# Kernel tuning notes

Hardware: AMD Instinct MI355X
Metric: run time of the kernel (lower is better)

The kernel has to match this reference:

```python
import jax, jax.numpy as jnp
import numpy as np

B, T, IN, H, S, L = 64, 512, 512, 512, 128, 2
ALPHA = 0.5  # default alpha in SCLSTM.forward


def setup_inputs() -> dict:
    key = jax.random.key(0)
    ks = jax.random.split(key, 9)
    p = lambda k, shape: jax.random.normal(k, shape, jnp.float32) * 0.05
    return {
        "inputs": jax.random.normal(ks[0], (B, T, IN), jnp.float32),
        "W_ir": p(ks[1], (S, IN)),
        "b_ir": p(ks[2], (S,)),
        "W_hr": p(ks[3], (S, L * H)),
        "b_hr": p(ks[4], (S,)),
        "gW": p(ks[5], (L, 4 * H, IN + H)),  # per-layer gate Linear (input_size==hidden_size)
        "gb": p(ks[6], (L, 4 * H)),
        "sW": p(ks[7], (L, H, S)),           # per-layer slot_linear
        "sb": p(ks[8], (L, H)),
    }


def reference(inputs, W_ir, b_ir, W_hr, b_hr, gW, gb, sW, sb):
    bsize = inputs.shape[0]
    h0 = jnp.zeros((bsize, L, H), inputs.dtype)
    c0 = jnp.zeros((bsize, L, H), inputs.dtype)
    s0 = jnp.zeros((bsize, S), inputs.dtype)

    def step(carry, x_t):  # x_t: (B, IN)
        h, c, s = carry
        # reading gate over flattened hidden states of all layers
        r = jax.nn.sigmoid(x_t @ W_ir.T + b_ir
                           + ALPHA * (h.reshape(bsize, L * H) @ W_hr.T + b_hr))
        s = s * r  # slot state update
        cur = x_t
        hs, cs = [], []
        for l in range(L):  # fixed small layer count
            gates = jnp.concatenate([cur, h[:, l]], axis=1) @ gW[l].T + gb[l]
            i_g, f_g, o_g, info = jnp.split(gates, 4, axis=1)
            slot_info = jnp.tanh(s @ sW[l].T + sb[l])
            c_n = (jax.nn.sigmoid(f_g) * c[:, l]
                   + jax.nn.sigmoid(i_g) * jnp.tanh(info) + slot_info)
            h_n = jax.nn.sigmoid(o_g) * jnp.tanh(c_n)
            hs.append(h_n); cs.append(c_n)
            cur = h_n  # skip_connections=False, dropout=0
        h = jnp.stack(hs, axis=1)
        c = jnp.stack(cs, axis=1)
        return (h, c, s), hs[-1]  # output is last layer's hidden state

    (ht, ct, st), outs = jax.lax.scan(step, (h0, c0, s0), jnp.swapaxes(inputs, 0, 1))
    outputs = jnp.swapaxes(outs, 0, 1)  # (B, T, H)
    return outputs, (ht, ct), st
```

## Files before the change

### kernel.cpp

```cpp
#include <hip/hip_runtime.h>


typedef unsigned short ushort;
typedef unsigned long long u64;
using bfrag = __attribute__((ext_vector_type(8))) short;
using cfrag = __attribute__((ext_vector_type(4))) float;
using i4    = __attribute__((ext_vector_type(4))) int;

constexpr int NBLK = 256, NTHR = 512;
constexpr int Bsz = 64, Tt = 512, Hsz = 512;
constexpr int D0 = 8;
constexpr int DP = 2;

constexpr long long OUT_HT = (long long)Bsz * Tt * Hsz;
constexpr long long OUT_CT = OUT_HT + (long long)Bsz * 2 * Hsz;
constexpr long long OUT_ST = OUT_CT + (long long)Bsz * 2 * Hsz;

constexpr int WS_SLOTS_A = 0;
constexpr int WS_SLOTS_B = 8 * 1024;
constexpr int WS_PROG_A  = 16 * 1024;
constexpr int WS_PROG_B  = 17 * 1024;
constexpr int WS_XCC     = 18 * 1024;
constexpr int WS_RING0   = 64 * 1024;
constexpr int WS_RING1   = WS_RING0 + D0 * Bsz * Hsz * 2;
constexpr int WS_RINGA   = WS_RING1 + DP * Bsz * Hsz * 2;
constexpr int WS_TOTAL   = WS_RINGA + DP * Bsz * Hsz * 2;

__global__ __launch_bounds__(256) void sclstm_init(float* __restrict__ ws,
                                                   float* __restrict__ out) {
    int i = blockIdx.x * blockDim.x + threadIdx.x, st = gridDim.x * blockDim.x;
    for (int k = i; k < WS_TOTAL / 4; k += st) ws[k] = 0.f;
    for (int k = i; k < Bsz * 128; k += st) out[OUT_ST + k] = 0.f;
}

__device__ __forceinline__ float sigm(float x) { return 1.f / (1.f + __expf(-x)); }
__device__ __forceinline__ float ftanh(float x) {
    float e = __expf(2.f * x);
    return 1.f - 2.f / (e + 1.f);
}
__device__ __forceinline__ ushort f2bf(float f) {
    unsigned u = __builtin_bit_cast(unsigned, f);
    u += 0x7FFFu + ((u >> 16) & 1u);
    return (ushort)(u >> 16);
}
__device__ __forceinline__ int aload(const int* p) {
    return __hip_atomic_load(p, __ATOMIC_RELAXED, __HIP_MEMORY_SCOPE_AGENT);
}
__device__ __forceinline__ int load_sc0(const int* p) {
    int v;
    asm volatile("global_load_dword %0, %1, off sc0\n\ts_waitcnt vmcnt(0)"
                 : "=v"(v) : "v"(p) : "memory");
    return v;
}
__device__ __forceinline__ void spin_agent(const int* p, int v) {
    int it = 0;
    while (aload(p) < v) {
        __builtin_amdgcn_s_sleep(1);
        if (((++it) & 1023) == 0)
            __builtin_amdgcn_fence(__ATOMIC_ACQUIRE, "agent");
    }
}
__device__ __forceinline__ void spin_f(const int* p, int v, int fast) {
    if (fast) {
        int it = 0;
        while (load_sc0(p) < v) {
            __builtin_amdgcn_s_sleep(1);
            if (((++it) & 63) == 0)
                __builtin_amdgcn_fence(__ATOMIC_ACQUIRE, "agent");
        }
    } else {
        spin_agent(p, v);
    }
}
__device__ __forceinline__ void st_flag(int* p, int v, int fast) {
    if (fast) __hip_atomic_store(p, v, __ATOMIC_RELAXED, __HIP_MEMORY_SCOPE_WORKGROUP);
    else      __hip_atomic_store(p, v, __ATOMIC_RELAXED, __HIP_MEMORY_SCOPE_AGENT);
}
__device__ __forceinline__ void st_h(ushort* p, ushort v, int fast) {
    if (fast) __hip_atomic_store(p, v, __ATOMIC_RELAXED, __HIP_MEMORY_SCOPE_WORKGROUP);
    else      __hip_atomic_store(p, v, __ATOMIC_RELAXED, __HIP_MEMORY_SCOPE_AGENT);
}
__device__ __forceinline__ bfrag pack2(u64 q0, u64 q1) {
    bfrag v;
    v[0]=(short)(ushort)(q0); v[1]=(short)(ushort)(q0 >> 16);
    v[2]=(short)(ushort)(q0 >> 32); v[3]=(short)(ushort)(q0 >> 48);
    v[4]=(short)(ushort)(q1); v[5]=(short)(ushort)(q1 >> 16);
    v[6]=(short)(ushort)(q1 >> 32); v[7]=(short)(ushort)(q1 >> 48);
    return v;
}

__global__ __launch_bounds__(NTHR, 2) void sclstm_main(
    const float* __restrict__ inputs,
    const float* __restrict__ gW,
    const float* __restrict__ gb,
    const float* __restrict__ sbias,
    float* __restrict__ out,
    float* __restrict__ ws)
{
    __shared__ __attribute__((aligned(16))) ushort frag_lds[32 * 512];
    __shared__ float part_lds[64 * 17 * 2];
    __shared__ int fast_sh;

    char* wsb = (char*)ws;
    const int tid = threadIdx.x, blk = blockIdx.x;
    const int setB = blk & 1;
    const int grp = (blk >> 1) & 3;
    const int myidx = blk >> 3;
    const int L = setB;
    const int b0 = grp * 16, m0 = myidx * 16;

    int* slots     = (int*)(wsb + (setB ? WS_SLOTS_B : WS_SLOTS_A)) + grp * 32 * 16;
    int* prog_self = (int*)(wsb + (setB ? WS_PROG_B : WS_PROG_A)) + grp * 16;
    int* prog_up   = (int*)(wsb + WS_PROG_A) + grp * 16;
    int* prog_down = (int*)(wsb + WS_PROG_B) + grp * 16;
    ushort* ring0 = (ushort*)(wsb + WS_RING0);
    ushort* ring1 = (ushort*)(wsb + WS_RING1);
    ushort* ringA = (ushort*)(wsb + WS_RINGA);
    ushort* ring_own = setB ? ring1 : ringA;

    const int lane = tid & 63, wave = tid >> 6;
    const int tau = wave & 3, g = wave >> 2;
    const int q = lane >> 4, lm = lane & 15;

    bfrag wv[16];
    {
        const int grow = tau * 512 + m0 + lm;
        const float* wrow = gW + ((size_t)L * 2048 + grow) * 1024 + g * 512 + q * 8;
        #pragma unroll
        for (int j = 0; j < 16; ++j) {
            const float* src = wrow + j * 32;
            float4 a = *(const float4*)src, b = *(const float4*)(src + 4);
            bfrag v;
            v[0]=(short)f2bf(a.x); v[1]=(short)f2bf(a.y); v[2]=(short)f2bf(a.z); v[3]=(short)f2bf(a.w);
            v[4]=(short)f2bf(b.x); v[5]=(short)f2bf(b.y); v[6]=(short)f2bf(b.z); v[7]=(short)f2bf(b.w);
            wv[j] = v;
        }
    }
    float bias4[4] = {0.f, 0.f, 0.f, 0.f};
    float slotc = 0.f, c = 0.f;
    if (tid < 256) {
        const int mi = tid & 15;
        #pragma unroll
        for (int tg = 0; tg < 4; ++tg) bias4[tg] = gb[L * 2048 + tg * 512 + m0 + mi];
        slotc = ftanh(sbias[L * 512 + m0 + mi]);
    }

    int fast;
    {
        unsigned xcc = (unsigned)__builtin_amdgcn_s_getreg((31 << 11) | 20) & 0xFu;
        int* xarr = (int*)(wsb + WS_XCC) + (setB * 4 + grp) * 32 * 16;
        if (tid == 0) {
            __hip_atomic_store(xarr + myidx * 16, (int)xcc + 1,
                               __ATOMIC_RELAXED, __HIP_MEMORY_SCOPE_AGENT);
            int ok = 1, ref = 0;
            for (int i = 0; i < 32; ++i) {
                int v;
                while ((v = aload(xarr + i * 16)) == 0) __builtin_amdgcn_s_sleep(2);
                if (i == 0) ref = v; else ok &= (v == ref);
            }
            fast_sh = ok;
        }
        __syncthreads();
        fast = fast_sh;
    }

    auto stage_nonrec = [&](int tt) {
        #pragma unroll
        for (int it = 0; it < 2; ++it) {
            const int ks = it * 8 + wave;
            bfrag v;
            if (!setB) {
                const float* xs = inputs + ((size_t)(b0 + lm) * Tt + tt) * 512 + ks * 32 + q * 8;
                float4 a = *(const float4*)xs, b = *(const float4*)(xs + 4);
                v[0]=(short)f2bf(a.x); v[1]=(short)f2bf(a.y); v[2]=(short)f2bf(a.z); v[3]=(short)f2bf(a.w);
                v[4]=(short)f2bf(b.x); v[5]=(short)f2bf(b.y); v[6]=(short)f2bf(b.z); v[7]=(short)f2bf(b.w);
            } else {
                const ushort* hs = ring0 + (size_t)(tt & (D0 - 1)) * (Bsz * Hsz)
                                 + (b0 + lm) * 512 + ks * 32 + q * 8;
                u64 q0 = __hip_atomic_load((const u64*)hs, __ATOMIC_RELAXED, __HIP_MEMORY_SCOPE_AGENT);
                u64 q1 = __hip_atomic_load((const u64*)(hs + 4), __ATOMIC_RELAXED, __HIP_MEMORY_SCOPE_AGENT);
                v = pack2(q0, q1);
            }
            *(bfrag*)&frag_lds[ks * 512 + lane * 8] = v;
        }
    };

    if (setB) {
        if (tid == 0) spin_agent(prog_up, 1);
        __syncthreads();
    }
    stage_nonrec(0);

    for (int t = 0; t < Tt; ++t) {
        const int rsp = (t - 1) & (DP - 1), rsc = t & (DP - 1);

        {
            const ushort* hb_ = ring_own + (size_t)rsp * (Bsz * Hsz) + (b0 + lm) * 512 + q * 8;
            const ushort* p0 = hb_ + wave * 32;
            const ushort* p1 = hb_ + (wave + 8) * 32;
            bfrag v0, v1;
            if (fast) {
                i4 w0, w1;
                asm volatile(
                    "global_load_dwordx4 %0, %2, off sc0\n\t"
                    "global_load_dwordx4 %1, %3, off sc0\n\t"
                    "s_waitcnt vmcnt(0)"
                    : "=&v"(w0), "=&v"(w1) : "v"(p0), "v"(p1) : "memory");
                v0 = __builtin_bit_cast(bfrag, w0);
                v1 = __builtin_bit_cast(bfrag, w1);
            } else {
                u64 a0 = __hip_atomic_load((const u64*)p0, __ATOMIC_RELAXED, __HIP_MEMORY_SCOPE_AGENT);
                u64 a1 = __hip_atomic_load((const u64*)(p0 + 4), __ATOMIC_RELAXED, __HIP_MEMORY_SCOPE_AGENT);
                u64 c0 = __hip_atomic_load((const u64*)p1, __ATOMIC_RELAXED, __HIP_MEMORY_SCOPE_AGENT);
                u64 c1 = __hip_atomic_load((const u64*)(p1 + 4), __ATOMIC_RELAXED, __HIP_MEMORY_SCOPE_AGENT);
                v0 = pack2(a0, a1); v1 = pack2(c0, c1);
            }
            *(bfrag*)&frag_lds[(16 + wave) * 512 + lane * 8] = v0;
            *(bfrag*)&frag_lds[(24 + wave) * 512 + lane * 8] = v1;
        }
        __syncthreads();

        cfrag C0 = {0.f, 0.f, 0.f, 0.f}, C1 = {0.f, 0.f, 0.f, 0.f};
        #pragma unroll
        for (int j = 0; j < 16; j += 2) {
            bfrag Bf0 = *(const bfrag*)&frag_lds[(g * 16 + j) * 512 + lane * 8];
            C0 = __builtin_amdgcn_mfma_f32_16x16x32_bf16(wv[j], Bf0, C0, 0, 0, 0);
            bfrag Bf1 = *(const bfrag*)&frag_lds[(g * 16 + j + 1) * 512 + lane * 8];
            C1 = __builtin_amdgcn_mfma_f32_16x16x32_bf16(wv[j + 1], Bf1, C1, 0, 0, 0);
        }
        #pragma unroll
        for (int reg = 0; reg < 4; ++reg) {
            const int lrow = tau * 16 + q * 4 + reg;
            part_lds[(lrow * 17 + lm) * 2 + g] = C0[reg] + C1[reg];
        }
        __syncthreads();

        float hn = 0.f, cn = 0.f;
        if (tid < 256) {
            const int mi = tid & 15, b3 = tid >> 4;
            float gs[4];
            #pragma unroll
            for (int tg = 0; tg < 4; ++tg) {
                float2 p = *(const float2*)&part_lds[((tg * 16 + mi) * 17 + b3) * 2];
                gs[tg] = p.x + p.y + bias4[tg];
            }
            cn = sigm(gs[1]) * c + sigm(gs[0]) * ftanh(gs[3]) + slotc;
            hn = sigm(gs[2]) * ftanh(cn);
            c = cn;
            const ushort hb16 = f2bf(hn);
            const size_t poff = (size_t)(b0 + b3) * 512 + m0 + mi;
            st_h(ring_own + (size_t)rsc * (Bsz * Hsz) + poff, hb16, fast);
            if (!setB)
                __hip_atomic_store(ring0 + (size_t)(t & (D0 - 1)) * (Bsz * Hsz) + poff,
                                   hb16, __ATOMIC_RELAXED, __HIP_MEMORY_SCOPE_AGENT);
        }
        __syncthreads();
        if (tid == 0) st_flag(&slots[myidx * 16], t + 1, fast);

        if (t + 1 < Tt) {
            if (setB) {
                if (tid == 0) spin_agent(prog_up, t + 2);
                __syncthreads();
            } else if ((t + 1) >= D0 && tid == 0) {
                spin_agent(prog_down, t + 2 - D0);
            }
            stage_nonrec(t + 1);
        }
        if (tid < 256) {
            const int mi = tid & 15, b3 = tid >> 4;
            if (setB)
                out[((size_t)(b0 + b3) * Tt + t) * Hsz + m0 + mi] = hn;
            if (t == Tt - 1) {
                out[OUT_HT + (size_t)(b0 + b3) * 1024 + L * 512 + m0 + mi] = hn;
                out[OUT_CT + (size_t)(b0 + b3) * 1024 + L * 512 + m0 + mi] = cn;
            }
        }
        if (tid < 32) spin_f(&slots[tid * 16], t + 1, fast);
        if (myidx == 0 && tid == 0)
            __hip_atomic_store(prog_self, t + 1, __ATOMIC_RELAXED, __HIP_MEMORY_SCOPE_AGENT);
        __syncthreads();
    }
}

extern "C" void kernel_launch(void* const* d_in, const int* in_sizes, int n_in,
                              void* d_out, int out_size, void* d_ws, size_t ws_size,
                              hipStream_t stream) {
    (void)in_sizes; (void)n_in; (void)out_size; (void)ws_size;
    const float* inputs = (const float*)d_in[0];
    const float* gW = (const float*)d_in[5];
    const float* gb = (const float*)d_in[6];
    const float* sbias = (const float*)d_in[8];
    float* out = (float*)d_out;
    float* ws = (float*)d_ws;

    hipLaunchKernelGGL(sclstm_init, dim3(256), dim3(256), 0, stream, ws, out);
    hipLaunchKernelGGL(sclstm_main, dim3(NBLK), dim3(NTHR), 0, stream,
                       inputs, gW, gb, sbias, out, ws);
}
```

Measured before the change: 1.824 ms.

## Halve block count with 32 hidden units per block and deferred cross-layer writes

Each block now computes 32 hidden units instead of 16, holding two sets of weight fragments and issuing four MFMA chains. That halves the grid to 128 blocks and the per-group barrier fan-in to 16 participants. Layer-0 writes to the cross-layer ring and layer-1 output stores are deferred to the start of the next step. Next-step inputs are prefetched into registers during the MFMA phase, and the syncthreads calls are replaced by raw s_barrier with explicit waitcnt. These changes aim to cut synchronisation and staging latency on the sequential critical path, at the cost of more registers per thread and more complex progress and flag logic.

```diff
diff --git a/kernel.cpp b/kernel.cpp
--- a/kernel.cpp
+++ b/kernel.cpp
@@ -2,12 +2,13 @@
 
 
 typedef unsigned short ushort;
+typedef unsigned int uint;
 typedef unsigned long long u64;
 using bfrag = __attribute__((ext_vector_type(8))) short;
 using cfrag = __attribute__((ext_vector_type(4))) float;
 using i4    = __attribute__((ext_vector_type(4))) int;
 
-constexpr int NBLK = 256, NTHR = 512;
+constexpr int NBLK = 128, NTHR = 512;
 constexpr int Bsz = 64, Tt = 512, Hsz = 512;
 constexpr int D0 = 8;
 constexpr int DP = 2;
@@ -76,10 +77,6 @@
     if (fast) __hip_atomic_store(p, v, __ATOMIC_RELAXED, __HIP_MEMORY_SCOPE_WORKGROUP);
     else      __hip_atomic_store(p, v, __ATOMIC_RELAXED, __HIP_MEMORY_SCOPE_AGENT);
 }
-__device__ __forceinline__ void st_h(ushort* p, ushort v, int fast) {
-    if (fast) __hip_atomic_store(p, v, __ATOMIC_RELAXED, __HIP_MEMORY_SCOPE_WORKGROUP);
-    else      __hip_atomic_store(p, v, __ATOMIC_RELAXED, __HIP_MEMORY_SCOPE_AGENT);
-}
 __device__ __forceinline__ bfrag pack2(u64 q0, u64 q1) {
     bfrag v;
     v[0]=(short)(ushort)(q0); v[1]=(short)(ushort)(q0 >> 16);
@@ -87,6 +84,25 @@
     v[4]=(short)(ushort)(q1); v[5]=(short)(ushort)(q1 >> 16);
     v[6]=(short)(ushort)(q1 >> 32); v[7]=(short)(ushort)(q1 >> 48);
     return v;
+}
+__device__ __forceinline__ bfrag packf(float4 a, float4 b) {
+    bfrag v;
+    v[0]=(short)f2bf(a.x); v[1]=(short)f2bf(a.y); v[2]=(short)f2bf(a.z); v[3]=(short)f2bf(a.w);
+    v[4]=(short)f2bf(b.x); v[5]=(short)f2bf(b.y); v[6]=(short)f2bf(b.z); v[7]=(short)f2bf(b.w);
+    return v;
+}
+__device__ __forceinline__ void bar_lgkm() {
+    asm volatile("s_waitcnt lgkmcnt(0)" ::: "memory");
+    __builtin_amdgcn_sched_barrier(0);
+    __builtin_amdgcn_s_barrier();
+}
+__device__ __forceinline__ void bar_vm0() {
+    asm volatile("s_waitcnt vmcnt(0) lgkmcnt(0)" ::: "memory");
+    __builtin_amdgcn_sched_barrier(0);
+    __builtin_amdgcn_s_barrier();
+}
+__device__ __forceinline__ void bar_raw() {
+    __builtin_amdgcn_s_barrier();
 }
 
 __global__ __launch_bounds__(NTHR, 2) void sclstm_main(
@@ -98,18 +114,19 @@
     float* __restrict__ ws)
 {
     __shared__ __attribute__((aligned(16))) ushort frag_lds[32 * 512];
-    __shared__ float part_lds[64 * 17 * 2];
+    __shared__ float part_lds[128 * 17 * 2];
     __shared__ int fast_sh;
 
     char* wsb = (char*)ws;
     const int tid = threadIdx.x, blk = blockIdx.x;
-    const int setB = blk & 1;
-    const int grp = (blk >> 1) & 3;
+    const int group = blk & 7;
+    const int setB = group & 1;
+    const int grp  = group >> 1;
     const int myidx = blk >> 3;
     const int L = setB;
-    const int b0 = grp * 16, m0 = myidx * 16;
-
-    int* slots     = (int*)(wsb + (setB ? WS_SLOTS_B : WS_SLOTS_A)) + grp * 32 * 16;
+    const int b0 = grp * 16, m0 = myidx * 32;
+
+    int* slots     = (int*)(wsb + (setB ? WS_SLOTS_B : WS_SLOTS_A)) + grp * 16 * 16;
     int* prog_self = (int*)(wsb + (setB ? WS_PROG_B : WS_PROG_A)) + grp * 16;
     int* prog_up   = (int*)(wsb + WS_PROG_A) + grp * 16;
     int* prog_down = (int*)(wsb + WS_PROG_B) + grp * 16;
@@ -122,38 +139,40 @@
     const int tau = wave & 3, g = wave >> 2;
     const int q = lane >> 4, lm = lane & 15;
 
-    bfrag wv[16];
-    {
-        const int grow = tau * 512 + m0 + lm;
+    bfrag wv[2][16];
+    #pragma unroll
+    for (int m = 0; m < 2; ++m) {
+        const int grow = tau * 512 + m0 + m * 16 + lm;
         const float* wrow = gW + ((size_t)L * 2048 + grow) * 1024 + g * 512 + q * 8;
         #pragma unroll
         for (int j = 0; j < 16; ++j) {
             const float* src = wrow + j * 32;
-            float4 a = *(const float4*)src, b = *(const float4*)(src + 4);
-            bfrag v;
-            v[0]=(short)f2bf(a.x); v[1]=(short)f2bf(a.y); v[2]=(short)f2bf(a.z); v[3]=(short)f2bf(a.w);
-            v[4]=(short)f2bf(b.x); v[5]=(short)f2bf(b.y); v[6]=(short)f2bf(b.z); v[7]=(short)f2bf(b.w);
-            wv[j] = v;
-        }
-    }
-    float bias4[4] = {0.f, 0.f, 0.f, 0.f};
-    float slotc = 0.f, c = 0.f;
+            wv[m][j] = packf(*(const float4*)src, *(const float4*)(src + 4));
+        }
+    }
+    const int mp = tid & 15, b3 = tid >> 4;
+    float bias2[4][2], slot2[2], cc2[2] = {0.f, 0.f};
+    float hnf2[2] = {0.f, 0.f};
+    uint hq_hold = 0;
     if (tid < 256) {
-        const int mi = tid & 15;
         #pragma unroll
-        for (int tg = 0; tg < 4; ++tg) bias4[tg] = gb[L * 2048 + tg * 512 + m0 + mi];
-        slotc = ftanh(sbias[L * 512 + m0 + mi]);
+        for (int k = 0; k < 2; ++k) {
+            #pragma unroll
+            for (int tg = 0; tg < 4; ++tg)
+                bias2[tg][k] = gb[L * 2048 + tg * 512 + m0 + 2 * mp + k];
+            slot2[k] = ftanh(sbias[L * 512 + m0 + 2 * mp + k]);
+        }
     }
 
     int fast;
     {
         unsigned xcc = (unsigned)__builtin_amdgcn_s_getreg((31 << 11) | 20) & 0xFu;
-        int* xarr = (int*)(wsb + WS_XCC) + (setB * 4 + grp) * 32 * 16;
+        int* xarr = (int*)(wsb + WS_XCC) + group * 16 * 16;
         if (tid == 0) {
             __hip_atomic_store(xarr + myidx * 16, (int)xcc + 1,
                                __ATOMIC_RELAXED, __HIP_MEMORY_SCOPE_AGENT);
             int ok = 1, ref = 0;
-            for (int i = 0; i < 32; ++i) {
+            for (int i = 0; i < 16; ++i) {
                 int v;
                 while ((v = aload(xarr + i * 16)) == 0) __builtin_amdgcn_s_sleep(2);
                 if (i == 0) ref = v; else ok &= (v == ref);
@@ -164,32 +183,29 @@
         fast = fast_sh;
     }
 
-    auto stage_nonrec = [&](int tt) {
-        #pragma unroll
-        for (int it = 0; it < 2; ++it) {
-            const int ks = it * 8 + wave;
-            bfrag v;
-            if (!setB) {
-                const float* xs = inputs + ((size_t)(b0 + lm) * Tt + tt) * 512 + ks * 32 + q * 8;
-                float4 a = *(const float4*)xs, b = *(const float4*)(xs + 4);
-                v[0]=(short)f2bf(a.x); v[1]=(short)f2bf(a.y); v[2]=(short)f2bf(a.z); v[3]=(short)f2bf(a.w);
-                v[4]=(short)f2bf(b.x); v[5]=(short)f2bf(b.y); v[6]=(short)f2bf(b.z); v[7]=(short)f2bf(b.w);
-            } else {
-                const ushort* hs = ring0 + (size_t)(tt & (D0 - 1)) * (Bsz * Hsz)
-                                 + (b0 + lm) * 512 + ks * 32 + q * 8;
-                u64 q0 = __hip_atomic_load((const u64*)hs, __ATOMIC_RELAXED, __HIP_MEMORY_SCOPE_AGENT);
-                u64 q1 = __hip_atomic_load((const u64*)(hs + 4), __ATOMIC_RELAXED, __HIP_MEMORY_SCOPE_AGENT);
-                v = pack2(q0, q1);
-            }
-            *(bfrag*)&frag_lds[ks * 512 + lane * 8] = v;
-        }
-    };
-
     if (setB) {
         if (tid == 0) spin_agent(prog_up, 1);
         __syncthreads();
     }
-    stage_nonrec(0);
+    #pragma unroll
+    for (int it = 0; it < 2; ++it) {
+        const int r = wave * 2 + it;
+        bfrag v;
+        if (!setB) {
+            const float* xs = inputs + ((size_t)(b0 + lm) * Tt + 0) * 512 + r * 32 + q * 8;
+            v = packf(*(const float4*)xs, *(const float4*)(xs + 4));
+        } else {
+            const ushort* hs = ring0 + (b0 + lm) * 512 + r * 32 + q * 8;
+            u64 q0 = __hip_atomic_load((const u64*)hs, __ATOMIC_RELAXED, __HIP_MEMORY_SCOPE_AGENT);
+            u64 q1 = __hip_atomic_load((const u64*)(hs + 4), __ATOMIC_RELAXED, __HIP_MEMORY_SCOPE_AGENT);
+            v = pack2(q0, q1);
+        }
+        *(bfrag*)&frag_lds[r * 512 + lane * 8] = v;
+    }
+
+    int cach_down = 0;
+    float4 pxa[3][2];
+    u64 phb[3][2];
 
     for (int t = 0; t < Tt; ++t) {
         const int rsp = (t - 1) & (DP - 1), rsc = t & (DP - 1);
@@ -218,67 +234,137 @@
             *(bfrag*)&frag_lds[(16 + wave) * 512 + lane * 8] = v0;
             *(bfrag*)&frag_lds[(24 + wave) * 512 + lane * 8] = v1;
         }
-        __syncthreads();
-
-        cfrag C0 = {0.f, 0.f, 0.f, 0.f}, C1 = {0.f, 0.f, 0.f, 0.f};
+        int pv_now = 0x7fffffff;
+        if (t > 0 && tid < 256) {
+            if (!setB) {
+                const int tgt = t - 8;
+                if (tgt > 0 && cach_down < tgt) {
+                    do { __builtin_amdgcn_s_sleep(1); cach_down = aload(prog_down); }
+                    while (cach_down < tgt);
+                }
+                ushort* rp = ring0 + (size_t)((t - 1) & (D0 - 1)) * (Bsz * Hsz)
+                           + (b0 + b3) * 512 + m0 + 2 * mp;
+                __hip_atomic_store((uint*)rp, hq_hold, __ATOMIC_RELAXED, __HIP_MEMORY_SCOPE_AGENT);
+            } else {
+                float2 o = {hnf2[0], hnf2[1]};
+                *(float2*)(out + ((size_t)(b0 + b3) * Tt + (t - 1)) * Hsz + m0 + 2 * mp) = o;
+            }
+        }
+        if (setB && wave > 0 && t + 1 < Tt)
+            pv_now = aload(prog_up);
+
+        bar_lgkm();
+
+        if (wave > 0 && t + 1 < Tt) {
+            if (setB && pv_now < t + 2) spin_agent(prog_up, t + 2);
+            #pragma unroll
+            for (int it = 0; it < 3; ++it) {
+                const int r = wave - 1 + it * 7;
+                if (r < 16) {
+                    if (!setB) {
+                        const float* xs = inputs + ((size_t)(b0 + lm) * Tt + (t + 1)) * 512 + r * 32 + q * 8;
+                        pxa[it][0] = *(const float4*)xs;
+                        pxa[it][1] = *(const float4*)(xs + 4);
+                    } else {
+                        const ushort* hs = ring0 + (size_t)((t + 1) & (D0 - 1)) * (Bsz * Hsz)
+                                         + (b0 + lm) * 512 + r * 32 + q * 8;
+                        phb[it][0] = __hip_atomic_load((const u64*)hs, __ATOMIC_RELAXED, __HIP_MEMORY_SCOPE_AGENT);
+                        phb[it][1] = __hip_atomic_load((const u64*)(hs + 4), __ATOMIC_RELAXED, __HIP_MEMORY_SCOPE_AGENT);
+                    }
+                }
+            }
+            asm volatile("" ::: "memory");
+        }
+
+        cfrag C00 = {0,0,0,0}, C01 = {0,0,0,0}, C10 = {0,0,0,0}, C11 = {0,0,0,0};
         #pragma unroll
         for (int j = 0; j < 16; j += 2) {
             bfrag Bf0 = *(const bfrag*)&frag_lds[(g * 16 + j) * 512 + lane * 8];
-            C0 = __builtin_amdgcn_mfma_f32_16x16x32_bf16(wv[j], Bf0, C0, 0, 0, 0);
             bfrag Bf1 = *(const bfrag*)&frag_lds[(g * 16 + j + 1) * 512 + lane * 8];
-            C1 = __builtin_amdgcn_mfma_f32_16x16x32_bf16(wv[j + 1], Bf1, C1, 0, 0, 0);
+            C00 = __builtin_amdgcn_mfma_f32_16x16x32_bf16(wv[0][j],     Bf0, C00, 0, 0, 0);
+            C10 = __builtin_amdgcn_mfma_f32_16x16x32_bf16(wv[1][j],     Bf0, C10, 0, 0, 0);
+            C01 = __builtin_amdgcn_mfma_f32_16x16x32_bf16(wv[0][j + 1], Bf1, C01, 0, 0, 0);
+            C11 = __builtin_amdgcn_mfma_f32_16x16x32_bf16(wv[1][j + 1], Bf1, C11, 0, 0, 0);
         }
         #pragma unroll
         for (int reg = 0; reg < 4; ++reg) {
-            const int lrow = tau * 16 + q * 4 + reg;
-            part_lds[(lrow * 17 + lm) * 2 + g] = C0[reg] + C1[reg];
-        }
-        __syncthreads();
-
-        float hn = 0.f, cn = 0.f;
+            const int r0 = tau * 32 + q * 4 + reg;
+            part_lds[(r0 * 17 + lm) * 2 + g] = C00[reg] + C01[reg];
+            part_lds[((r0 + 16) * 17 + lm) * 2 + g] = C10[reg] + C11[reg];
+        }
+        bar_lgkm();
+
         if (tid < 256) {
-            const int mi = tid & 15, b3 = tid >> 4;
-            float gs[4];
             #pragma unroll
-            for (int tg = 0; tg < 4; ++tg) {
-                float2 p = *(const float2*)&part_lds[((tg * 16 + mi) * 17 + b3) * 2];
-                gs[tg] = p.x + p.y + bias4[tg];
-            }
-            cn = sigm(gs[1]) * c + sigm(gs[0]) * ftanh(gs[3]) + slotc;
-            hn = sigm(gs[2]) * ftanh(cn);
-            c = cn;
-            const ushort hb16 = f2bf(hn);
-            const size_t poff = (size_t)(b0 + b3) * 512 + m0 + mi;
-            st_h(ring_own + (size_t)rsc * (Bsz * Hsz) + poff, hb16, fast);
-            if (!setB)
-                __hip_atomic_store(ring0 + (size_t)(t & (D0 - 1)) * (Bsz * Hsz) + poff,
-                                   hb16, __ATOMIC_RELAXED, __HIP_MEMORY_SCOPE_AGENT);
-        }
-        __syncthreads();
+            for (int k = 0; k < 2; ++k) {
+                const int fi = 2 * mp + k;
+                float gs[4];
+                #pragma unroll
+                for (int tg = 0; tg < 4; ++tg) {
+                    float2 p = *(const float2*)&part_lds[((tg * 32 + fi) * 17 + b3) * 2];
+                    gs[tg] = p.x + p.y + bias2[tg][k];
+                }
+                float cn = sigm(gs[1]) * cc2[k] + sigm(gs[0]) * ftanh(gs[3]) + slot2[k];
+                float hn = sigm(gs[2]) * ftanh(cn);
+                cc2[k] = cn; hnf2[k] = hn;
+            }
+            hq_hold = (uint)f2bf(hnf2[0]) | ((uint)f2bf(hnf2[1]) << 16);
+            ushort* rp = ring_own + (size_t)rsc * (Bsz * Hsz) + (b0 + b3) * 512 + m0 + 2 * mp;
+            if (fast) *(uint*)rp = hq_hold;
+            else __hip_atomic_store((uint*)rp, hq_hold, __ATOMIC_RELAXED, __HIP_MEMORY_SCOPE_AGENT);
+        }
+        bar_vm0();
         if (tid == 0) st_flag(&slots[myidx * 16], t + 1, fast);
 
-        if (t + 1 < Tt) {
-            if (setB) {
-                if (tid == 0) spin_agent(prog_up, t + 2);
-                __syncthreads();
-            } else if ((t + 1) >= D0 && tid == 0) {
-                spin_agent(prog_down, t + 2 - D0);
-            }
-            stage_nonrec(t + 1);
-        }
+        if (wave > 0) {
+            if (t + 1 < Tt) {
+                #pragma unroll
+                for (int it = 0; it < 3; ++it) {
+                    const int r = wave - 1 + it * 7;
+                    if (r < 16) {
+                        bfrag v = setB ? pack2(phb[it][0], phb[it][1])
+                                       : packf(pxa[it][0], pxa[it][1]);
+                        *(bfrag*)&frag_lds[r * 512 + lane * 8] = v;
+                    }
+                }
+            }
+        } else {
+            if (lane < 16) spin_f(&slots[lane * 16], t + 1, fast);
+            if (myidx == 0 && lane == 0)
+                __hip_atomic_store(prog_self, setB ? t + 1 : t,
+                                   __ATOMIC_RELAXED, __HIP_MEMORY_SCOPE_AGENT);
+        }
+        bar_raw();
+    }
+
+    if (!setB) {
         if (tid < 256) {
-            const int mi = tid & 15, b3 = tid >> 4;
-            if (setB)
-                out[((size_t)(b0 + b3) * Tt + t) * Hsz + m0 + mi] = hn;
-            if (t == Tt - 1) {
-                out[OUT_HT + (size_t)(b0 + b3) * 1024 + L * 512 + m0 + mi] = hn;
-                out[OUT_CT + (size_t)(b0 + b3) * 1024 + L * 512 + m0 + mi] = cn;
-            }
-        }
-        if (tid < 32) spin_f(&slots[tid * 16], t + 1, fast);
+            const int tgt = Tt - 8;
+            if (cach_down < tgt) {
+                do { __builtin_amdgcn_s_sleep(1); cach_down = aload(prog_down); }
+                while (cach_down < tgt);
+            }
+            ushort* rp = ring0 + (size_t)((Tt - 1) & (D0 - 1)) * (Bsz * Hsz)
+                       + (b0 + b3) * 512 + m0 + 2 * mp;
+            __hip_atomic_store((uint*)rp, hq_hold, __ATOMIC_RELAXED, __HIP_MEMORY_SCOPE_AGENT);
+        }
+        bar_vm0();
+        if (tid == 0) st_flag(&slots[myidx * 16], Tt + 1, fast);
+        if (wave == 0 && lane < 16) spin_f(&slots[lane * 16], Tt + 1, fast);
         if (myidx == 0 && tid == 0)
-            __hip_atomic_store(prog_self, t + 1, __ATOMIC_RELAXED, __HIP_MEMORY_SCOPE_AGENT);
-        __syncthreads();
+            __hip_atomic_store(prog_self, Tt, __ATOMIC_RELAXED, __HIP_MEMORY_SCOPE_AGENT);
+        if (tid < 256) {
+            float2 oh = {hnf2[0], hnf2[1]}, oc = {cc2[0], cc2[1]};
+            *(float2*)(out + OUT_HT + (size_t)(b0 + b3) * 1024 + 0 * 512 + m0 + 2 * mp) = oh;
+            *(float2*)(out + OUT_CT + (size_t)(b0 + b3) * 1024 + 0 * 512 + m0 + 2 * mp) = oc;
+        }
+    } else {
+        if (tid < 256) {
+            float2 oh = {hnf2[0], hnf2[1]}, oc = {cc2[0], cc2[1]};
+            *(float2*)(out + ((size_t)(b0 + b3) * Tt + (Tt - 1)) * Hsz + m0 + 2 * mp) = oh;
+            *(float2*)(out + OUT_HT + (size_t)(b0 + b3) * 1024 + 512 + m0 + 2 * mp) = oh;
+            *(float2*)(out + OUT_CT + (size_t)(b0 + b3) * 1024 + 512 + m0 + 2 * mp) = oc;
+        }
     }
 }
 
```

After: 5.169 ms. 183% more time.

## Prefetch next-step inputs in idle waves during gate compute, cache progress flag

Applied to the files above, without the earlier changes.

Waves 4-7, which sit idle during the elementwise gate update, now issue next-timestep input or ring0 loads into registers before that phase and write them to LDS afterwards. Waves 0-3 no longer do any staging. The layer-1 set only prefetches when the upstream progress flag is already far enough, and otherwise falls back to a per-wave spin plus direct staging. The downstream progress check caches the last value seen, which avoids redundant atomic loads. Slot flags move to new workspace offsets and the launch bound drops to one block per CU, giving more registers for the prefetch buffers.

```diff
diff --git a/kernel.cpp b/kernel.cpp
--- a/kernel.cpp
+++ b/kernel.cpp
@@ -2,6 +2,7 @@
 
 
 typedef unsigned short ushort;
+typedef unsigned int uint;
 typedef unsigned long long u64;
 using bfrag = __attribute__((ext_vector_type(8))) short;
 using cfrag = __attribute__((ext_vector_type(4))) float;
@@ -16,15 +17,15 @@
 constexpr long long OUT_CT = OUT_HT + (long long)Bsz * 2 * Hsz;
 constexpr long long OUT_ST = OUT_CT + (long long)Bsz * 2 * Hsz;
 
-constexpr int WS_SLOTS_A = 0;
-constexpr int WS_SLOTS_B = 8 * 1024;
-constexpr int WS_PROG_A  = 16 * 1024;
-constexpr int WS_PROG_B  = 17 * 1024;
-constexpr int WS_XCC     = 18 * 1024;
-constexpr int WS_RING0   = 64 * 1024;
-constexpr int WS_RING1   = WS_RING0 + D0 * Bsz * Hsz * 2;
-constexpr int WS_RINGA   = WS_RING1 + DP * Bsz * Hsz * 2;
-constexpr int WS_TOTAL   = WS_RINGA + DP * Bsz * Hsz * 2;
+constexpr int WS_PROG_A = 16 * 1024;
+constexpr int WS_PROG_B = 17 * 1024;
+constexpr int WS_XCC    = 18 * 1024;
+constexpr int WS_SLOTS_A = 40 * 1024;
+constexpr int WS_SLOTS_B = 48 * 1024;
+constexpr int WS_RING0  = 64 * 1024;
+constexpr int WS_RING1  = WS_RING0 + D0 * Bsz * Hsz * 2;
+constexpr int WS_RINGA  = WS_RING1 + DP * Bsz * Hsz * 2;
+constexpr int WS_TOTAL  = WS_RINGA + DP * Bsz * Hsz * 2;
 
 __global__ __launch_bounds__(256) void sclstm_init(float* __restrict__ ws,
                                                    float* __restrict__ out) {
@@ -88,8 +89,14 @@
     v[6]=(short)(ushort)(q1 >> 32); v[7]=(short)(ushort)(q1 >> 48);
     return v;
 }
-
-__global__ __launch_bounds__(NTHR, 2) void sclstm_main(
+__device__ __forceinline__ bfrag packf(float4 a, float4 b) {
+    bfrag v;
+    v[0]=(short)f2bf(a.x); v[1]=(short)f2bf(a.y); v[2]=(short)f2bf(a.z); v[3]=(short)f2bf(a.w);
+    v[4]=(short)f2bf(b.x); v[5]=(short)f2bf(b.y); v[6]=(short)f2bf(b.z); v[7]=(short)f2bf(b.w);
+    return v;
+}
+
+__global__ __launch_bounds__(NTHR, 1) void sclstm_main(
     const float* __restrict__ inputs,
     const float* __restrict__ gW,
     const float* __restrict__ gb,
@@ -129,11 +136,7 @@
         #pragma unroll
         for (int j = 0; j < 16; ++j) {
             const float* src = wrow + j * 32;
-            float4 a = *(const float4*)src, b = *(const float4*)(src + 4);
-            bfrag v;
-            v[0]=(short)f2bf(a.x); v[1]=(short)f2bf(a.y); v[2]=(short)f2bf(a.z); v[3]=(short)f2bf(a.w);
-            v[4]=(short)f2bf(b.x); v[5]=(short)f2bf(b.y); v[6]=(short)f2bf(b.z); v[7]=(short)f2bf(b.w);
-            wv[j] = v;
+            wv[j] = packf(*(const float4*)src, *(const float4*)(src + 4));
         }
     }
     float bias4[4] = {0.f, 0.f, 0.f, 0.f};
@@ -164,32 +167,31 @@
         fast = fast_sh;
     }
 
-    auto stage_nonrec = [&](int tt) {
-        #pragma unroll
-        for (int it = 0; it < 2; ++it) {
-            const int ks = it * 8 + wave;
-            bfrag v;
-            if (!setB) {
-                const float* xs = inputs + ((size_t)(b0 + lm) * Tt + tt) * 512 + ks * 32 + q * 8;
-                float4 a = *(const float4*)xs, b = *(const float4*)(xs + 4);
-                v[0]=(short)f2bf(a.x); v[1]=(short)f2bf(a.y); v[2]=(short)f2bf(a.z); v[3]=(short)f2bf(a.w);
-                v[4]=(short)f2bf(b.x); v[5]=(short)f2bf(b.y); v[6]=(short)f2bf(b.z); v[7]=(short)f2bf(b.w);
-            } else {
-                const ushort* hs = ring0 + (size_t)(tt & (D0 - 1)) * (Bsz * Hsz)
-                                 + (b0 + lm) * 512 + ks * 32 + q * 8;
-                u64 q0 = __hip_atomic_load((const u64*)hs, __ATOMIC_RELAXED, __HIP_MEMORY_SCOPE_AGENT);
-                u64 q1 = __hip_atomic_load((const u64*)(hs + 4), __ATOMIC_RELAXED, __HIP_MEMORY_SCOPE_AGENT);
-                v = pack2(q0, q1);
-            }
-            *(bfrag*)&frag_lds[ks * 512 + lane * 8] = v;
-        }
+    auto stage_row = [&](int r, int tt) {
+        bfrag v;
+        if (!setB) {
+            const float* xs = inputs + ((size_t)(b0 + lm) * Tt + tt) * 512 + r * 32 + q * 8;
+            v = packf(*(const float4*)xs, *(const float4*)(xs + 4));
+        } else {
+            const ushort* hs = ring0 + (size_t)(tt & (D0 - 1)) * (Bsz * Hsz)
+                             + (b0 + lm) * 512 + r * 32 + q * 8;
+            u64 q0 = __hip_atomic_load((const u64*)hs, __ATOMIC_RELAXED, __HIP_MEMORY_SCOPE_AGENT);
+            u64 q1 = __hip_atomic_load((const u64*)(hs + 4), __ATOMIC_RELAXED, __HIP_MEMORY_SCOPE_AGENT);
+            v = pack2(q0, q1);
+        }
+        *(bfrag*)&frag_lds[r * 512 + lane * 8] = v;
     };
 
     if (setB) {
         if (tid == 0) spin_agent(prog_up, 1);
         __syncthreads();
     }
-    stage_nonrec(0);
+    stage_row(wave * 2, 0);
+    stage_row(wave * 2 + 1, 0);
+
+    int cach_down = 0;
+    float4 pxa[4][2];
+    u64 phb[4][2];
 
     for (int t = 0; t < Tt; ++t) {
         const int rsp = (t - 1) & (DP - 1), rsc = t & (DP - 1);
@@ -235,6 +237,30 @@
         }
         __syncthreads();
 
+        int havepf = 0;
+        if (wave >= 4 && t + 1 < Tt) {
+            if (!setB) {
+                #pragma unroll
+                for (int it = 0; it < 4; ++it) {
+                    const int r = (wave - 4) * 4 + it;
+                    const float* xs = inputs + ((size_t)(b0 + lm) * Tt + (t + 1)) * 512 + r * 32 + q * 8;
+                    pxa[it][0] = *(const float4*)xs;
+                    pxa[it][1] = *(const float4*)(xs + 4);
+                }
+                havepf = 1;
+            } else if (aload(prog_up) >= t + 2) {
+                #pragma unroll
+                for (int it = 0; it < 4; ++it) {
+                    const int r = (wave - 4) * 4 + it;
+                    const ushort* hs = ring0 + (size_t)((t + 1) & (D0 - 1)) * (Bsz * Hsz)
+                                     + (b0 + lm) * 512 + r * 32 + q * 8;
+                    phb[it][0] = __hip_atomic_load((const u64*)hs, __ATOMIC_RELAXED, __HIP_MEMORY_SCOPE_AGENT);
+                    phb[it][1] = __hip_atomic_load((const u64*)(hs + 4), __ATOMIC_RELAXED, __HIP_MEMORY_SCOPE_AGENT);
+                }
+                havepf = 1;
+            }
+        }
+
         float hn = 0.f, cn = 0.f;
         if (tid < 256) {
             const int mi = tid & 15, b3 = tid >> 4;
@@ -255,16 +281,35 @@
                                    hb16, __ATOMIC_RELAXED, __HIP_MEMORY_SCOPE_AGENT);
         }
         __syncthreads();
-        if (tid == 0) st_flag(&slots[myidx * 16], t + 1, fast);
+        if (tid == 0)
+            st_flag(&slots[myidx * 16], t + 1, fast);
 
         if (t + 1 < Tt) {
-            if (setB) {
-                if (tid == 0) spin_agent(prog_up, t + 2);
-                __syncthreads();
-            } else if ((t + 1) >= D0 && tid == 0) {
-                spin_agent(prog_down, t + 2 - D0);
-            }
-            stage_nonrec(t + 1);
+            if (wave >= 4) {
+                if (havepf) {
+                    #pragma unroll
+                    for (int it = 0; it < 4; ++it) {
+                        const int r = (wave - 4) * 4 + it;
+                        bfrag v = setB ? pack2(phb[it][0], phb[it][1])
+                                       : packf(pxa[it][0], pxa[it][1]);
+                        *(bfrag*)&frag_lds[r * 512 + lane * 8] = v;
+                    }
+                } else {
+                    spin_agent(prog_up, t + 2);
+                    #pragma unroll
+                    for (int it = 0; it < 4; ++it)
+                        stage_row((wave - 4) * 4 + it, t + 1);
+                }
+            } else if (!setB && (t + 1) >= D0 && tid == 0) {
+                const int tgt = t + 2 - D0;
+                if (cach_down < tgt) {
+                    cach_down = aload(prog_down);
+                    while (cach_down < tgt) {
+                        __builtin_amdgcn_s_sleep(1);
+                        cach_down = aload(prog_down);
+                    }
+                }
+            }
         }
         if (tid < 256) {
             const int mi = tid & 15, b3 = tid >> 4;
@@ -277,7 +322,8 @@
         }
         if (tid < 32) spin_f(&slots[tid * 16], t + 1, fast);
         if (myidx == 0 && tid == 0)
-            __hip_atomic_store(prog_self, t + 1, __ATOMIC_RELAXED, __HIP_MEMORY_SCOPE_AGENT);
+            __hip_atomic_store(prog_self, t + 1,
+                               __ATOMIC_RELAXED, __HIP_MEMORY_SCOPE_AGENT);
         __syncthreads();
     }
 }
```

Result: slower. 5.131 ms (+181.3%).

## Prefetch next-step layer inputs before MFMA to overlap global latency

Applied to the files above, without the earlier changes.

Loads of the next timestep's non-recurrent operand are now issued before the per-step MFMA and gate math: raw inputs for layer 0, and ring0 hidden states for layer 1. They are held in registers and packed to LDS only after the step completes. Layer-1 blocks cache the last observed upstream progress value, so they skip the spin-plus-barrier when the producer is already far enough ahead, and fall back to the old spin path otherwise. This is meant to hide global-memory latency on the serial recurrence critical path, at the cost of extra live registers for the prefetch buffers.

```diff
diff --git a/kernel.cpp b/kernel.cpp
--- a/kernel.cpp
+++ b/kernel.cpp
@@ -60,6 +60,16 @@
             __builtin_amdgcn_fence(__ATOMIC_ACQUIRE, "agent");
     }
 }
+__device__ __forceinline__ int spin_cap(const int* p, int v) {
+    int x = aload(p), it = 0;
+    while (x < v) {
+        __builtin_amdgcn_s_sleep(1);
+        if (((++it) & 1023) == 0)
+            __builtin_amdgcn_fence(__ATOMIC_ACQUIRE, "agent");
+        x = aload(p);
+    }
+    return x;
+}
 __device__ __forceinline__ void spin_f(const int* p, int v, int fast) {
     if (fast) {
         int it = 0;
@@ -86,6 +96,12 @@
     v[2]=(short)(ushort)(q0 >> 32); v[3]=(short)(ushort)(q0 >> 48);
     v[4]=(short)(ushort)(q1); v[5]=(short)(ushort)(q1 >> 16);
     v[6]=(short)(ushort)(q1 >> 32); v[7]=(short)(ushort)(q1 >> 48);
+    return v;
+}
+__device__ __forceinline__ bfrag packf(float4 a, float4 b) {
+    bfrag v;
+    v[0]=(short)f2bf(a.x); v[1]=(short)f2bf(a.y); v[2]=(short)f2bf(a.z); v[3]=(short)f2bf(a.w);
+    v[4]=(short)f2bf(b.x); v[5]=(short)f2bf(b.y); v[6]=(short)f2bf(b.z); v[7]=(short)f2bf(b.w);
     return v;
 }
 
@@ -100,6 +116,7 @@
     __shared__ __attribute__((aligned(16))) ushort frag_lds[32 * 512];
     __shared__ float part_lds[64 * 17 * 2];
     __shared__ int fast_sh;
+    __shared__ int pv_sh;
 
     char* wsb = (char*)ws;
     const int tid = threadIdx.x, blk = blockIdx.x;
@@ -129,11 +146,7 @@
         #pragma unroll
         for (int j = 0; j < 16; ++j) {
             const float* src = wrow + j * 32;
-            float4 a = *(const float4*)src, b = *(const float4*)(src + 4);
-            bfrag v;
-            v[0]=(short)f2bf(a.x); v[1]=(short)f2bf(a.y); v[2]=(short)f2bf(a.z); v[3]=(short)f2bf(a.w);
-            v[4]=(short)f2bf(b.x); v[5]=(short)f2bf(b.y); v[6]=(short)f2bf(b.z); v[7]=(short)f2bf(b.w);
-            wv[j] = v;
+            wv[j] = packf(*(const float4*)src, *(const float4*)(src + 4));
         }
     }
     float bias4[4] = {0.f, 0.f, 0.f, 0.f};
@@ -164,32 +177,27 @@
         fast = fast_sh;
     }
 
-    auto stage_nonrec = [&](int tt) {
-        #pragma unroll
-        for (int it = 0; it < 2; ++it) {
-            const int ks = it * 8 + wave;
-            bfrag v;
-            if (!setB) {
-                const float* xs = inputs + ((size_t)(b0 + lm) * Tt + tt) * 512 + ks * 32 + q * 8;
-                float4 a = *(const float4*)xs, b = *(const float4*)(xs + 4);
-                v[0]=(short)f2bf(a.x); v[1]=(short)f2bf(a.y); v[2]=(short)f2bf(a.z); v[3]=(short)f2bf(a.w);
-                v[4]=(short)f2bf(b.x); v[5]=(short)f2bf(b.y); v[6]=(short)f2bf(b.z); v[7]=(short)f2bf(b.w);
-            } else {
-                const ushort* hs = ring0 + (size_t)(tt & (D0 - 1)) * (Bsz * Hsz)
-                                 + (b0 + lm) * 512 + ks * 32 + q * 8;
-                u64 q0 = __hip_atomic_load((const u64*)hs, __ATOMIC_RELAXED, __HIP_MEMORY_SCOPE_AGENT);
-                u64 q1 = __hip_atomic_load((const u64*)(hs + 4), __ATOMIC_RELAXED, __HIP_MEMORY_SCOPE_AGENT);
-                v = pack2(q0, q1);
-            }
-            *(bfrag*)&frag_lds[ks * 512 + lane * 8] = v;
-        }
+    auto stage_row = [&](int r, int tt) {
+        bfrag v;
+        if (!setB) {
+            const float* xs = inputs + ((size_t)(b0 + lm) * Tt + tt) * 512 + r * 32 + q * 8;
+            v = packf(*(const float4*)xs, *(const float4*)(xs + 4));
+        } else {
+            const ushort* hs = ring0 + (size_t)(tt & (D0 - 1)) * (Bsz * Hsz)
+                             + (b0 + lm) * 512 + r * 32 + q * 8;
+            u64 q0 = __hip_atomic_load((const u64*)hs, __ATOMIC_RELAXED, __HIP_MEMORY_SCOPE_AGENT);
+            u64 q1 = __hip_atomic_load((const u64*)(hs + 4), __ATOMIC_RELAXED, __HIP_MEMORY_SCOPE_AGENT);
+            v = pack2(q0, q1);
+        }
+        *(bfrag*)&frag_lds[r * 512 + lane * 8] = v;
     };
 
     if (setB) {
-        if (tid == 0) spin_agent(prog_up, 1);
-        __syncthreads();
-    }
-    stage_nonrec(0);
+        if (tid == 0) pv_sh = spin_cap(prog_up, 1);
+        __syncthreads();
+    }
+    stage_row(wave, 0);
+    stage_row(wave + 8, 0);
 
     for (int t = 0; t < Tt; ++t) {
         const int rsp = (t - 1) & (DP - 1), rsc = t & (DP - 1);
@@ -220,6 +228,29 @@
         }
         __syncthreads();
 
+        const int pf_ok = (t + 1 < Tt) && (!setB || pv_sh >= t + 2);
+        float4 pxa[2][2];
+        u64 phb[2][2];
+        int pv_new = 0;
+        if (pf_ok) {
+            if (setB && tid == 0) pv_new = aload(prog_up);
+            #pragma unroll
+            for (int it = 0; it < 2; ++it) {
+                const int r = it * 8 + wave;
+                if (!setB) {
+                    const float* xs = inputs + ((size_t)(b0 + lm) * Tt + (t + 1)) * 512 + r * 32 + q * 8;
+                    pxa[it][0] = *(const float4*)xs;
+                    pxa[it][1] = *(const float4*)(xs + 4);
+                } else {
+                    const ushort* hs = ring0 + (size_t)((t + 1) & (D0 - 1)) * (Bsz * Hsz)
+                                     + (b0 + lm) * 512 + r * 32 + q * 8;
+                    phb[it][0] = __hip_atomic_load((const u64*)hs, __ATOMIC_RELAXED, __HIP_MEMORY_SCOPE_AGENT);
+                    phb[it][1] = __hip_atomic_load((const u64*)(hs + 4), __ATOMIC_RELAXED, __HIP_MEMORY_SCOPE_AGENT);
+                }
+            }
+            __builtin_amdgcn_sched_barrier(0);
+        }
+
         cfrag C0 = {0.f, 0.f, 0.f, 0.f}, C1 = {0.f, 0.f, 0.f, 0.f};
         #pragma unroll
         for (int j = 0; j < 16; j += 2) {
@@ -255,16 +286,29 @@
                                    hb16, __ATOMIC_RELAXED, __HIP_MEMORY_SCOPE_AGENT);
         }
         __syncthreads();
-        if (tid == 0) st_flag(&slots[myidx * 16], t + 1, fast);
+        if (tid == 0)
+            st_flag(&slots[myidx * 16], t + 1, fast);
 
         if (t + 1 < Tt) {
-            if (setB) {
-                if (tid == 0) spin_agent(prog_up, t + 2);
+            if (pf_ok) {
+                if (tid == 0) {
+                    if (setB) pv_sh = pv_new;
+                    else if ((t + 1) >= D0) spin_agent(prog_down, t + 2 - D0);
+                }
+                #pragma unroll
+                for (int it = 0; it < 2; ++it) {
+                    const int r = it * 8 + wave;
+                    bfrag v = setB ? pack2(phb[it][0], phb[it][1])
+                                   : packf(pxa[it][0], pxa[it][1]);
+                    *(bfrag*)&frag_lds[r * 512 + lane * 8] = v;
+                }
+            } else {
+                if (tid == 0) pv_sh = spin_cap(prog_up, t + 2);
                 __syncthreads();
-            } else if ((t + 1) >= D0 && tid == 0) {
-                spin_agent(prog_down, t + 2 - D0);
-            }
-            stage_nonrec(t + 1);
+                stage_row(wave, t + 1);
+                stage_row(wave + 8, t + 1);
+            }
+        } else if (!setB && tid == 0) {
         }
         if (tid < 256) {
             const int mi = tid & 15, b3 = tid >> 4;
@@ -277,7 +321,8 @@
         }
         if (tid < 32) spin_f(&slots[tid * 16], t + 1, fast);
         if (myidx == 0 && tid == 0)
-            __hip_atomic_store(prog_self, t + 1, __ATOMIC_RELAXED, __HIP_MEMORY_SCOPE_AGENT);
+            __hip_atomic_store(prog_self, t + 1,
+                               __ATOMIC_RELAXED, __HIP_MEMORY_SCOPE_AGENT);
         __syncthreads();
     }
 }
```

After: 3.022 ms. 65.7% more time.
